# Kernel tuning notes

Measured on AMD Instinct MI355X. Metric: run time of the kernel, lower is better.

The kernel has to match this reference:

```python
import jax, jax.numpy as jnp
import numpy as np
import math

NEG = -1e9


def maximum_path(neg_cent, text_len, spec_len):
    # neg_cent: [B, Ts, Tt]; monotonic alignment (Viterbi) DP as in VITS.
    B, Ts, Tt = neg_cent.shape
    jj = jnp.arange(Tt)
    tt = jnp.arange(Ts)
    node_mask = (jj[None, None, :] < text_len[:, None, None]) & (tt[None, :, None] < spec_len[:, None, None])
    nc = jnp.where(node_mask, neg_cent, NEG)

    def fstep(q, nc_t):
        # q: [B, Tt] best score ending at text index j at previous frame
        q_shift = jnp.concatenate([jnp.full((B, 1), NEG, q.dtype), q[:, :-1]], axis=1)
        d = q_shift >= q  # True -> came from j-1 (diagonal move)
        q_new = nc_t + jnp.maximum(q, q_shift)
        return q_new, d

    q0 = jnp.broadcast_to(jnp.where(jj == 0, 0.0, NEG), (B, Tt)).astype(neg_cent.dtype)
    _, dirs = jax.lax.scan(fstep, q0, jnp.swapaxes(nc, 0, 1))  # dirs: [Ts, B, Tt]

    def bstep(j, inp):
        t, d_t = inp
        start = (t == spec_len - 1)
        j_eff = jnp.where(start, text_len - 1, j)
        valid = t < spec_len
        emit = ((jj[None, :] == j_eff[:, None]) & valid[:, None]).astype(neg_cent.dtype)
        came_diag = jnp.take_along_axis(d_t, j_eff[:, None], axis=1)[:, 0]
        j_next = jnp.where(valid, jnp.maximum(j_eff - came_diag.astype(j_eff.dtype), 0), j_eff)
        return j_next, emit

    j_init = jnp.zeros((B,), text_len.dtype)
    _, path = jax.lax.scan(bstep, j_init, (jnp.arange(Ts), dirs), reverse=True)
    return jnp.swapaxes(path, 0, 1)  # [B, Ts, Tt]


def setup_inputs() -> dict:
    B, C, Ts, Tt = 16, 192, 2048, 512
    key = jax.random.key(0)
    k1, k2, k3, k4, k5 = jax.random.split(key, 5)
    z_p = jax.random.normal(k1, (B, C, Ts), dtype=jnp.float32)
    m_p = jax.random.normal(k2, (B, C, Tt), dtype=jnp.float32)
    logs_p = 0.1 * jax.random.normal(k3, (B, C, Tt), dtype=jnp.float32)
    text_len = jax.random.randint(k4, (B,), Tt // 2, Tt + 1, dtype=jnp.int32)
    extra = jax.random.randint(k5, (B,), 0, Ts - Tt + 1, dtype=jnp.int32)
    spec_len = jnp.minimum(text_len + extra, Ts)
    return {"z_p": z_p, "m_p": m_p, "logs_p": logs_p, "spec_len": spec_len, "text_len": text_len}


def reference(z_p, m_p, logs_p, spec_len, text_len):
    B, C, Ts = z_p.shape
    Tt = m_p.shape[2]
    text_mask = (jnp.arange(Tt)[None, :] < text_len[:, None]).astype(z_p.dtype)[:, None, :]  # [B,1,Tt]
    spec_mask = (jnp.arange(Ts)[None, :] < spec_len[:, None]).astype(z_p.dtype)[:, None, :]  # [B,1,Ts]

    # --- neg_cent (torch.no_grad block) ---
    s_p_sq_r = jnp.exp(-2.0 * logs_p)  # [B,C,Tt]
    neg_cent1 = jnp.sum(-0.5 * math.log(2.0 * math.pi) - logs_p, axis=1, keepdims=True)  # [B,1,Tt]
    neg_cent2 = jnp.einsum('bct,bcu->btu', -0.5 * z_p ** 2, s_p_sq_r)  # [B,Ts,Tt]
    neg_cent3 = jnp.einsum('bct,bcu->btu', z_p, m_p * s_p_sq_r)  # [B,Ts,Tt]
    neg_cent4 = jnp.sum(-0.5 * m_p ** 2 * s_p_sq_r, axis=1, keepdims=True)  # [B,1,Tt]
    neg_cent = neg_cent1 + neg_cent2 + neg_cent3 + neg_cent4

    path = jax.lax.stop_gradient(maximum_path(neg_cent, text_len, spec_len))  # [B,Ts,Tt]

    duration = jnp.sum(path, axis=1)[:, None, :]  # [B,1,Tt]
    logw_ = jnp.log(duration + 1e-6) * text_mask  # [B,1,Tt]

    # expand prior stats along the alignment path: [B,C,Ts]
    m_p_exp = jnp.einsum('btu,bcu->bct', path, m_p)
    logs_p_exp = jnp.einsum('btu,bcu->bct', path, logs_p)

    return (path, duration, logw_, m_p_exp, logs_p_exp, text_mask, spec_mask)
```

## Files before the change

kernel.cpp:

```cpp
#include <hip/hip_runtime.h>
#include <hip/hip_bf16.h>
#include <math.h>

#define BB 16
#define CC 192
#define TS 2048
#define TT 512
#define KK 384

#define OFF_PATH 0
#define OFF_DUR  (16777216)
#define OFF_LOGW (OFF_DUR + 8192)
#define OFF_MEXP (OFF_LOGW + 8192)
#define OFF_LEXP (OFF_MEXP + 6291456)
#define OFF_TMASK (OFF_LEXP + 6291456)
#define OFF_SMASK (OFF_TMASK + 8192)

#define NEGCF (-1e9f)

__global__ __launch_bounds__(512) void vits_prep(
    const float* __restrict__ m_p, const float* __restrict__ logs_p,
    const int* __restrict__ spec_len, const int* __restrict__ text_len,
    float* __restrict__ Bmat, float* __restrict__ avec,
    float* __restrict__ tmask, float* __restrict__ smask)
{
    const int uc = blockIdx.x;
    const int b  = blockIdx.y;
    const int tid = threadIdx.x;
    const int ul = tid & 31;
    const int cg = tid >> 5;
    const int u = uc*32 + ul;
    const float C0 = -0.91893853320467274178f;
    float a_acc = 0.f;
    for (int c = cg; c < CC; c += 16) {
        float lg = logs_p[((size_t)b*CC + c)*TT + u];
        float mm = m_p[((size_t)b*CC + c)*TT + u];
        float s  = expf(-2.f*lg);
        float ms = mm * s;
        Bmat[((size_t)b*KK + 2*c    )*TT + u] = ms;
        Bmat[((size_t)b*KK + 2*c + 1)*TT + u] = s;
        a_acc += C0 - lg - 0.5f*mm*ms;
    }
    __shared__ float red[16][33];
    red[cg][ul] = a_acc;
    __syncthreads();
    #pragma unroll
    for (int s = 8; s > 0; s >>= 1) {
        if (cg < s) red[cg][ul] += red[cg + s][ul];
        __syncthreads();
    }
    if (cg == 0) {
        avec[b*TT + u] = red[0][ul];
        tmask[b*TT + u] = (u < text_len[b]) ? 1.f : 0.f;
    }
    if (tid < 128) {
        int t = uc*128 + tid;
        smask[b*TS + t] = (t < spec_len[b]) ? 1.f : 0.f;
    }
}

__global__ __launch_bounds__(256) void vits_gemm(
    const float* __restrict__ z, const float* __restrict__ Bmat,
    const float* __restrict__ avec, float* __restrict__ out)
{
    const int b  = blockIdx.z;
    const int t0 = blockIdx.y * 64;
    const int u0 = blockIdx.x * 64;
    __shared__ float As[16][68];
    __shared__ float Bs[16][68];
    const int tid = threadIdx.x;
    const int tx = tid & 15, ty = tid >> 4;
    float acc[4][4] = {};
    const float* zb = z    + (size_t)b * CC * TS;
    const float* Bb = Bmat + (size_t)b * KK * TT;
    for (int kc = 0; kc < KK/16; ++kc) {
        {
            int c_l = tid >> 5;
            int t_l = (tid & 31) * 2;
            const float* zp = zb + (size_t)(kc*8 + c_l)*TS + t0 + t_l;
            float2 zv = *(const float2*)zp;
            float2 z1 = make_float2(zv.x, zv.y);
            float2 z2 = make_float2(-0.5f*zv.x*zv.x, -0.5f*zv.y*zv.y);
            *(float2*)&As[2*c_l  ][t_l] = z1;
            *(float2*)&As[2*c_l+1][t_l] = z2;
            int k_l = tid >> 4;
            int u_l = (tid & 15) * 4;
            const float* bp = Bb + (size_t)(kc*16 + k_l)*TT + u0 + u_l;
            *(float4*)&Bs[k_l][u_l] = *(const float4*)bp;
        }
        __syncthreads();
        #pragma unroll
        for (int kk = 0; kk < 16; ++kk) {
            float4 av = *(const float4*)&As[kk][ty*4];
            float4 bv = *(const float4*)&Bs[kk][tx*4];
            float aa[4] = {av.x, av.y, av.z, av.w};
            float bb[4] = {bv.x, bv.y, bv.z, bv.w};
            #pragma unroll
            for (int i = 0; i < 4; ++i)
                #pragma unroll
                for (int jj = 0; jj < 4; ++jj)
                    acc[i][jj] += aa[i]*bb[jj];
        }
        __syncthreads();
    }
    float4 a4 = *(const float4*)(avec + b*TT + u0 + tx*4);
    float ab[4] = {a4.x, a4.y, a4.z, a4.w};
    #pragma unroll
    for (int i = 0; i < 4; ++i) {
        float4 o;
        o.x = acc[i][0] + ab[0];
        o.y = acc[i][1] + ab[1];
        o.z = acc[i][2] + ab[2];
        o.w = acc[i][3] + ab[3];
        *(float4*)(out + ((size_t)b*TS + t0 + ty*4 + i)*TT + u0 + tx*4) = o;
    }
}

__device__ __forceinline__ float dpp_ror1_f32(float v) {
    union { float f; int i; } u, r;
    u.f = v;
    r.i = __builtin_amdgcn_update_dpp(0, u.i, 0x13C, 0xF, 0xF, false);
    return r.f;
}

#define DIRS(j,w) dirs[((j)<<6) | ((w) ^ ((j) & 31))]
#define RING 16

__global__ __launch_bounds__(1024, 1) void vits_dp(
    const float* __restrict__ nc,
    const int* __restrict__ spec_len, const int* __restrict__ text_len,
    float* __restrict__ dur, float* __restrict__ logw, int* __restrict__ jt)
{
    __shared__ unsigned int dirs[TT*(TS/32)];
    __shared__ float qrow[TT];
    __shared__ int Tr[TT + 1];

    const int tid  = threadIdx.x;
    const int lane = tid & 63;
    const int wid  = tid >> 6;
    const int b = blockIdx.x;
    const int SL = spec_len[b], TL = text_len[b];
    const int col = (wid << 5) + lane - 32;
    const bool auth = (lane >= 32);
    const bool w0g  = (wid == 0) && (lane < 32);
    const int colL = (col < 0) ? 0 : col;

    float q = (col == 0) ? 0.0f : NEGCF;
    unsigned int bits = 0;

    const float* ncb = nc + (size_t)b*TS*TT + colL;

    float pf[RING];
    #pragma unroll
    for (int i = 0; i < RING; ++i) pf[i] = ncb[(size_t)i*TT];
    const float* pcur = ncb + (size_t)RING*TT;

    int tb = 0;
    for (; tb + 32 <= SL; tb += 32) {
        #pragma unroll
        for (int s = 0; s < 32; ++s) {
            const int t = tb + s;
            float f = pf[s & (RING-1)];
            pf[s & (RING-1)] = *pcur;
            pcur += TT;

            float qp = dpp_ror1_f32(q);
            bool d = (qp >= q);
            bits = (bits << 1) | (unsigned)d;
            float qn = f + fmaxf(qp, q);
            q = w0g ? NEGCF : qn;

            if (s == 31) {
                if (auth) {
                    DIRS(col, t >> 5) = bits;
                    qrow[col] = q;
                }
                bits = 0;
                __syncthreads();
                if (!auth && wid != 0) q = qrow[col];
                __syncthreads();
            }
        }
    }
    for (int t = tb; t < SL; ++t) {
        float f = ncb[(size_t)t*TT];
        float qp = dpp_ror1_f32(q);
        bool d = (qp >= q);
        bits = (bits << 1) | (unsigned)d;
        float qn = f + fmaxf(qp, q);
        q = w0g ? NEGCF : qn;
    }
    if (SL & 31) {
        int w = SL >> 5, r = SL & 31;
        if (auth) DIRS(col, w) = bits << (32 - r);
    }
    __syncthreads();

    for (int i = tid; i <= TT; i += 1024) Tr[i] = 0;
    __syncthreads();

    if (tid == 0) {
        Tr[TL] = SL;
        int j = TL - 1, tc = SL - 1;
        while (j > 0 && tc >= 0) {
            int w = tc >> 5;
            int bcur = 31 - (tc & 31);
            unsigned int W = DIRS(j, w) & (0xFFFFFFFFu << bcur);
            if (W) {
                int bp = __ffs(W) - 1;
                int tp = (w << 5) + 31 - bp;
                Tr[j] = tp;
                --j;
                tc = tp - 1;
            } else {
                if (w == 0) break;
                tc = (w << 5) - 1;
            }
        }
    }
    __syncthreads();

    for (int u = tid; u < TT; u += 1024) {
        float dv = (u < TL) ? (float)(Tr[u+1] - Tr[u]) : 0.0f;
        dur[b*TT + u] = dv;
        logw[b*TT + u] = (u < TL) ? logf(dv + 1e-6f) : 0.0f;
    }
    for (int u = 0; u < TL; ++u) {
        int t1 = Tr[u+1];
        for (int t = Tr[u] + tid; t < t1; t += 1024) jt[b*TS + t] = u;
    }
    for (int t = SL + tid; t < TS; t += 1024) jt[b*TS + t] = -1;
}

__global__ void vits_path(const int* __restrict__ jt, float4* __restrict__ path)
{
    int idx = blockIdx.x*blockDim.x + threadIdx.x;
    const int total = BB*TS*(TT/4);
    for (; idx < total; idx += gridDim.x*blockDim.x) {
        int u4 = idx & (TT/4 - 1);
        int bt = idx >> 7;
        int j = jt[bt];
        float4 v = make_float4(0.f,0.f,0.f,0.f);
        int r = j - (u4 << 2);
        if (r >= 0 && r < 4) ((float*)&v)[r] = 1.f;
        path[idx] = v;
    }
}

__global__ void vits_mlexp(const int* __restrict__ jt,
    const float* __restrict__ m_p, const float* __restrict__ logs_p,
    float4* __restrict__ mexp, float4* __restrict__ lexp)
{
    int idx = blockIdx.x*blockDim.x + threadIdx.x;
    const int total = BB*CC*(TS/4);
    for (; idx < total; idx += gridDim.x*blockDim.x) {
        int t4 = idx & (TS/4 - 1);
        int bc = idx >> 9;
        int b = bc / CC;
        int4 jv = *(const int4*)(jt + b*TS + (t4 << 2));
        const float* mrow = m_p    + (size_t)bc*TT;
        const float* lrow = logs_p + (size_t)bc*TT;
        float4 mv, lv;
        mv.x = (jv.x >= 0) ? mrow[jv.x] : 0.f;  lv.x = (jv.x >= 0) ? lrow[jv.x] : 0.f;
        mv.y = (jv.y >= 0) ? mrow[jv.y] : 0.f;  lv.y = (jv.y >= 0) ? lrow[jv.y] : 0.f;
        mv.z = (jv.z >= 0) ? mrow[jv.z] : 0.f;  lv.z = (jv.z >= 0) ? lrow[jv.z] : 0.f;
        mv.w = (jv.w >= 0) ? mrow[jv.w] : 0.f;  lv.w = (jv.w >= 0) ? lrow[jv.w] : 0.f;
        mexp[idx] = mv;
        lexp[idx] = lv;
    }
}

extern "C" void kernel_launch(void* const* d_in, const int* in_sizes, int n_in,
                              void* d_out, int out_size, void* d_ws, size_t ws_size,
                              hipStream_t stream) {
    const float* z_p      = (const float*)d_in[0];
    const float* m_p      = (const float*)d_in[1];
    const float* logs_p   = (const float*)d_in[2];
    const int*   spec_len = (const int*)d_in[3];
    const int*   text_len = (const int*)d_in[4];
    float* out = (float*)d_out;

    float* Bmat = (float*)d_ws;
    float* avec = Bmat + (size_t)BB*KK*TT;
    int*   jt   = (int*)(avec + BB*TT);

    float* path  = out + OFF_PATH;
    float* dur   = out + OFF_DUR;
    float* logw  = out + OFF_LOGW;
    float* mexp  = out + OFF_MEXP;
    float* lexp  = out + OFF_LEXP;
    float* tmask = out + OFF_TMASK;
    float* smask = out + OFF_SMASK;

    vits_prep<<<dim3(16, BB), 512, 0, stream>>>(m_p, logs_p, spec_len, text_len,
                                                Bmat, avec, tmask, smask);
    vits_gemm<<<dim3(TT/64, TS/64, BB), 256, 0, stream>>>(z_p, Bmat, avec, path);
    vits_dp<<<BB, 1024, 0, stream>>>(path, spec_len, text_len, dur, logw, jt);
    vits_path<<<2048, 256, 0, stream>>>(jt, (float4*)path);
    vits_mlexp<<<2048, 256, 0, stream>>>(jt, m_p, logs_p, (float4*)mexp, (float4*)lexp);
}
```

Baseline: 461.2 us.

## Enlarge GEMM tile to 128x128 with 8x8 per-thread blocking and register prefetch

The neg_cent GEMM moves from 64x64 block tiles with 4x4 register micro-tiles to 128x128 block tiles with 8x8 micro-tiles over a K chunk of 8. The next chunk of global z and Bmat data is prefetched into registers while the current shared-memory chunk is computed. This raises arithmetic intensity per shared-memory load and hides global latency. The cost is higher register pressure and fewer blocks, which can lower occupancy.

After: 440.8 us. -4.4%, faster.

```diff
diff --git a/kernel.cpp b/kernel.cpp
--- a/kernel.cpp
+++ b/kernel.cpp
@@ -64,55 +64,64 @@
     const float* __restrict__ avec, float* __restrict__ out)
 {
     const int b  = blockIdx.z;
-    const int t0 = blockIdx.y * 64;
-    const int u0 = blockIdx.x * 64;
-    __shared__ float As[16][68];
-    __shared__ float Bs[16][68];
+    const int t0 = blockIdx.y * 128;
+    const int u0 = blockIdx.x * 128;
+    __shared__ float As[8][128];
+    __shared__ float Bs[8][128];
     const int tid = threadIdx.x;
     const int tx = tid & 15, ty = tid >> 4;
-    float acc[4][4] = {};
+    float acc[8][8] = {};
     const float* zb = z    + (size_t)b * CC * TS;
     const float* Bb = Bmat + (size_t)b * KK * TT;
-    for (int kc = 0; kc < KK/16; ++kc) {
-        {
-            int c_l = tid >> 5;
-            int t_l = (tid & 31) * 2;
-            const float* zp = zb + (size_t)(kc*8 + c_l)*TS + t0 + t_l;
-            float2 zv = *(const float2*)zp;
-            float2 z1 = make_float2(zv.x, zv.y);
-            float2 z2 = make_float2(-0.5f*zv.x*zv.x, -0.5f*zv.y*zv.y);
-            *(float2*)&As[2*c_l  ][t_l] = z1;
-            *(float2*)&As[2*c_l+1][t_l] = z2;
-            int k_l = tid >> 4;
-            int u_l = (tid & 15) * 4;
-            const float* bp = Bb + (size_t)(kc*16 + k_l)*TT + u0 + u_l;
-            *(float4*)&Bs[k_l][u_l] = *(const float4*)bp;
+
+    const int c_l = tid >> 6;
+    const int t_l = (tid & 63) * 2;
+    const int k_b = tid >> 5;
+    const int u_l = (tid & 31) * 4;
+
+    float2 zr = *(const float2*)(zb + (size_t)c_l*TS + t0 + t_l);
+    float4 br = *(const float4*)(Bb + (size_t)k_b*TT + u0 + u_l);
+
+    for (int kc = 0; kc < KK/8; ++kc) {
+        *(float2*)&As[2*c_l  ][t_l] = make_float2(zr.x, zr.y);
+        *(float2*)&As[2*c_l+1][t_l] = make_float2(-0.5f*zr.x*zr.x, -0.5f*zr.y*zr.y);
+        *(float4*)&Bs[k_b][u_l] = br;
+        __syncthreads();
+        if (kc + 1 < KK/8) {
+            zr = *(const float2*)(zb + (size_t)((kc+1)*4 + c_l)*TS + t0 + t_l);
+            br = *(const float4*)(Bb + (size_t)((kc+1)*8 + k_b)*TT + u0 + u_l);
+        }
+        #pragma unroll
+        for (int k = 0; k < 8; ++k) {
+            float4 a0 = *(const float4*)&As[k][ty*4];
+            float4 a1 = *(const float4*)&As[k][ty*4 + 64];
+            float4 b0 = *(const float4*)&Bs[k][tx*4];
+            float4 b1 = *(const float4*)&Bs[k][tx*4 + 64];
+            float aa[8] = {a0.x,a0.y,a0.z,a0.w,a1.x,a1.y,a1.z,a1.w};
+            float bb[8] = {b0.x,b0.y,b0.z,b0.w,b1.x,b1.y,b1.z,b1.w};
+            #pragma unroll
+            for (int i = 0; i < 8; ++i)
+                #pragma unroll
+                for (int j = 0; j < 8; ++j)
+                    acc[i][j] += aa[i]*bb[j];
         }
         __syncthreads();
-        #pragma unroll
-        for (int kk = 0; kk < 16; ++kk) {
-            float4 av = *(const float4*)&As[kk][ty*4];
-            float4 bv = *(const float4*)&Bs[kk][tx*4];
-            float aa[4] = {av.x, av.y, av.z, av.w};
-            float bb[4] = {bv.x, bv.y, bv.z, bv.w};
-            #pragma unroll
-            for (int i = 0; i < 4; ++i)
-                #pragma unroll
-                for (int jj = 0; jj < 4; ++jj)
-                    acc[i][jj] += aa[i]*bb[jj];
-        }
-        __syncthreads();
-    }
-    float4 a4 = *(const float4*)(avec + b*TT + u0 + tx*4);
-    float ab[4] = {a4.x, a4.y, a4.z, a4.w};
+    }
+
+    float4 ab0 = *(const float4*)(avec + b*TT + u0 + tx*4);
+    float4 ab1 = *(const float4*)(avec + b*TT + u0 + tx*4 + 64);
+    float ab[8] = {ab0.x,ab0.y,ab0.z,ab0.w,ab1.x,ab1.y,ab1.z,ab1.w};
     #pragma unroll
-    for (int i = 0; i < 4; ++i) {
-        float4 o;
-        o.x = acc[i][0] + ab[0];
-        o.y = acc[i][1] + ab[1];
-        o.z = acc[i][2] + ab[2];
-        o.w = acc[i][3] + ab[3];
-        *(float4*)(out + ((size_t)b*TS + t0 + ty*4 + i)*TT + u0 + tx*4) = o;
+    for (int i = 0; i < 8; ++i) {
+        int tt = t0 + ((i < 4) ? (ty*4 + i) : (64 + ty*4 + (i-4)));
+        float* orow = out + (size_t)((size_t)b*TS + tt)*TT + u0;
+        float4 o0, o1;
+        o0.x = acc[i][0] + ab[0]; o0.y = acc[i][1] + ab[1];
+        o0.z = acc[i][2] + ab[2]; o0.w = acc[i][3] + ab[3];
+        o1.x = acc[i][4] + ab[4]; o1.y = acc[i][5] + ab[5];
+        o1.z = acc[i][6] + ab[6]; o1.w = acc[i][7] + ab[7];
+        *(float4*)(orow + tx*4)      = o0;
+        *(float4*)(orow + tx*4 + 64) = o1;
     }
 }
 
@@ -294,7 +303,7 @@
 
     vits_prep<<<dim3(16, BB), 512, 0, stream>>>(m_p, logs_p, spec_len, text_len,
                                                 Bmat, avec, tmask, smask);
-    vits_gemm<<<dim3(TT/64, TS/64, BB), 256, 0, stream>>>(z_p, Bmat, avec, path);
+    vits_gemm<<<dim3(TT/128, TS/128, BB), 256, 0, stream>>>(z_p, Bmat, avec, path);
     vits_dp<<<BB, 1024, 0, stream>>>(path, spec_len, text_len, dur, logw, jt);
     vits_path<<<2048, 256, 0, stream>>>(jt, (float4*)path);
     vits_mlexp<<<2048, 256, 0, stream>>>(jt, m_p, logs_p, (float4*)mexp, (float4*)lexp);
```
